# Performance work log

Hardware: AMD Instinct MI355X
Metric: run time of the kernel (lower is better)

## Reference

```python
import jax, jax.numpy as jnp
import numpy as np

EPS = 1e-5
K = 5  # sklearn NearestNeighbors(n_neighbors=5); includes the query point itself


def setup_inputs() -> dict:
    key = jax.random.key(0)
    points = jax.random.uniform(key, (16384, 3), dtype=jnp.float32)
    return {"points": points}


def _compute_lrfs(points):
    # Brute-force KNN (indices only; sklearn returns the self-point as nearest).
    sq = jnp.sum(points * points, axis=1)                      # [N]
    d2 = sq[:, None] + sq[None, :] - 2.0 * points @ points.T   # [N,N]
    _, nbh_idx = jax.lax.top_k(-jax.lax.stop_gradient(d2), K)  # [N,K] (indices only -> no grad path)

    diffs = points[nbh_idx] - points[:, None, :]               # [N,K,3]  (nbh = points[idx] - point)
    centered = diffs - diffs.mean(axis=1, keepdims=True)
    cov = jnp.einsum('nkd,nke->nde', centered, centered) / K   # torch.cov(nbh.T, correction=0)
    eigvals, eigvecs = jnp.linalg.eigh(cov)                    # ascending eigvals, [N,3],[N,3,3]
    order = jnp.argsort(eigvals, axis=-1)[:, ::-1]             # descending

    # NOTE faithful quirks of the original:
    #  - eigvecs.T[:, axis] == eigvecs[axis, :] -> ROW of eigvecs is used as the axis
    #  - _calc_axis receives nbh (already point-relative) and does (pt - point) again,
    #    so the vote uses (neighbor - 2*point) dotted with the axis.
    def axis_row(idx):
        v = jnp.take_along_axis(eigvecs, idx[:, None, None], axis=1)[:, 0, :]  # [N,3]
        vote_vec = diffs - points[:, None, :]                                  # [N,K,3]
        count = jnp.sum(jnp.einsum('nkd,nd->nk', vote_vec, v) >= -EPS, axis=1)
        sign = jnp.where(2 * count >= K, 1.0, -1.0).astype(points.dtype)       # count >= K/2 keeps
        return v * sign[:, None]

    x_axis = axis_row(order[:, 0])
    z_axis = axis_row(order[:, 2])
    y_axis = jnp.cross(z_axis, x_axis)
    return jnp.stack([x_axis, y_axis, z_axis], axis=1)  # [N,3,3]


def reference(points):
    # forward(points, return_lrfs=True) -> (shot=0, lrfs); return the lrfs (the only real output).
    return _compute_lrfs(points)
```

## Files before the change

kernel.cpp:

```cpp
#include <hip/hip_runtime.h>

#define SLARTG_NEW 1

namespace {

constexpr int KNN_K = 5;
constexpr int GRID = 16;
constexpr int CELLS = GRID * GRID * GRID;
constexpr int LPG = 8;

constexpr int PPB = 16;
constexpr int STR = 16;
constexpr int TPB = PPB * STR;
constexpr int TILE = 2048;

#define EPSF    5.9604644775390625e-8f
#define EPS2F   3.552713678800501e-15f
#define SAFMINF 1.1754943508222875e-38f
#define SAFMAXF 8.507059173023462e+37f
#define RTMINF  1.0842021724855044e-19f
#define RTMAXF  9.223372036854776e+18f

__device__ __forceinline__ float sqnorm3(float x, float y, float z) {
#pragma clang fp contract(off)
  float a = x * x;
  float b = y * y;
  float c = z * z;
  return (a + b) + c;
}

__device__ __forceinline__ float dist2(float xi, float yi, float zi, float sqi,
                                       float xj, float yj, float zj, float sqj) {
#pragma clang fp contract(off)
  float dot = (xi * xj + yi * yj) + zi * zj;
  float a = sqi + sqj;
  return a - 2.0f * dot;
}

__device__ __forceinline__ int cell1d(float v) {
  int c = (int)(v * (float)GRID);
  if (c < 0) c = 0;
  if (c > GRID - 1) c = GRID - 1;
  return c;
}

__device__ __forceinline__ float slapy2f(float x, float y) {
#pragma clang fp contract(off)
  float xa = fabsf(x), ya = fabsf(y);
  float w = fmaxf(xa, ya);
  float z = fminf(xa, ya);
  if (z == 0.f) return w;
  float q = z / w;
  float q2 = q * q;
  float s = 1.0f + q2;
  return w * sqrtf(s);
}

__device__ __forceinline__ void slartgf(float f, float g, float* cs, float* sn, float* r) {
#pragma clang fp contract(off)
#if SLARTG_NEW
  float f1 = fabsf(f), g1 = fabsf(g);
  if (g == 0.f) { *cs = 1.f; *sn = 0.f; *r = f; }
  else if (f == 0.f) { *cs = 0.f; *sn = copysignf(1.f, g); *r = g1; }
  else if (f1 > RTMINF && f1 < RTMAXF && g1 > RTMINF && g1 < RTMAXF) {
    float ff = f * f;
    float gg = g * g;
    float d = sqrtf(ff + gg);
    *cs = f1 / d;
    float rr = copysignf(d, f);
    *sn = g / rr;
    *r = rr;
  } else {
    float u = fminf(SAFMAXF, fmaxf(fmaxf(SAFMINF, f1), g1));
    float fs = f / u, gs = g / u;
    float ff = fs * fs;
    float gg = gs * gs;
    float d = sqrtf(ff + gg);
    *cs = fabsf(fs) / d;
    float rr = copysignf(d, f);
    *sn = gs / rr;
    *r = rr * u;
  }
#else
  if (g == 0.f) { *cs = 1.f; *sn = 0.f; *r = f; }
  else if (f == 0.f) { *cs = 0.f; *sn = 1.f; *r = g; }
  else {
    float f2 = f * f;
    float g2 = g * g;
    float rr = sqrtf(f2 + g2);
    float c = f / rr, s = g / rr;
    if (fabsf(f) > fabsf(g) && c < 0.f) { c = -c; s = -s; rr = -rr; }
    *cs = c; *sn = s; *r = rr;
  }
#endif
}

__device__ __forceinline__ void slaev2f(float a, float b, float c,
                                        float* rt1, float* rt2, float* cs1, float* sn1) {
#pragma clang fp contract(off)
  float sm = a + c;
  float df = a - c;
  float adf = fabsf(df);
  float tb = b + b;
  float ab = fabsf(tb);
  float acmx, acmn;
  if (fabsf(a) > fabsf(c)) { acmx = a; acmn = c; } else { acmx = c; acmn = a; }
  float rt;
  if (adf > ab) { float q = ab / adf; rt = adf * sqrtf(1.0f + q * q); }
  else if (adf < ab) { float q = adf / ab; rt = ab * sqrtf(1.0f + q * q); }
  else rt = ab * sqrtf(2.0f);
  int sgn1;
  if (sm < 0.f) { *rt1 = 0.5f * (sm - rt); sgn1 = -1; *rt2 = (acmx / *rt1) * acmn - (b / *rt1) * b; }
  else if (sm > 0.f) { *rt1 = 0.5f * (sm + rt); sgn1 = 1; *rt2 = (acmx / *rt1) * acmn - (b / *rt1) * b; }
  else { *rt1 = 0.5f * rt; *rt2 = -0.5f * rt; sgn1 = 1; }
  float cs; int sgn2;
  if (df >= 0.f) { cs = df + rt; sgn2 = 1; } else { cs = df - rt; sgn2 = -1; }
  float acs = fabsf(cs);
  float c1, s1;
  if (acs > ab) {
    float ct = -tb / cs;
    s1 = 1.0f / sqrtf(1.0f + ct * ct);
    c1 = ct * s1;
  } else {
    if (ab == 0.f) { c1 = 1.f; s1 = 0.f; }
    else {
      float tn = -cs / tb;
      c1 = 1.0f / sqrtf(1.0f + tn * tn);
      s1 = tn * c1;
    }
  }
  if (sgn1 == sgn2) { float tn = c1; c1 = -s1; s1 = tn; }
  *cs1 = c1; *sn1 = s1;
}

__device__ __forceinline__ void slascl_g(float cfrom, float cto, int n, float* a) {
#pragma clang fp contract(off)
  float cfromc = cfrom, ctoc = cto;
  bool done = false;
  int guard = 0;
  while (!done && guard++ < 50) {
    float mul;
    float cfrom1 = cfromc * SAFMINF;
    if (cfrom1 == cfromc) {
      mul = ctoc / cfromc; done = true;
    } else {
      float cto1 = ctoc / SAFMAXF;
      if (cto1 == ctoc) { mul = ctoc; done = true; cfromc = 1.f; }
      else if (fabsf(cfrom1) > fabsf(ctoc) && ctoc != 0.f) { mul = SAFMINF; done = false; cfromc = cfrom1; }
      else if (fabsf(cto1) > fabsf(cfromc)) { mul = SAFMAXF; done = false; ctoc = cto1; }
      else { mul = ctoc / cfromc; done = true; }
    }
    for (int i = 0; i < n; ++i) a[i] = a[i] * mul;
  }
}

__device__ void steqr3f(float* d, float* e, float Z[3][3]) {
#pragma clang fp contract(off)
  const int n = 3;
  const float eps = EPSF, eps2 = EPS2F, safmin = SAFMINF;
  const float ssfmax = sqrtf(SAFMAXF) / 3.0f;
  const float ssfmin = sqrtf(SAFMINF) / EPS2F;
  int jtot = 0; const int nmaxit = n * 30;
  int l1 = 1;

  for (int guard = 0; guard < 200; ++guard) {
    if (l1 > n) break;
    if (l1 > 1) e[l1 - 2] = 0.f;
    int m = n;
    if (l1 <= n - 1) {
      for (int q = l1; q <= n - 1; ++q) {
        float tst = fabsf(e[q - 1]);
        if (tst == 0.f) { m = q; break; }
        if (tst <= (sqrtf(fabsf(d[q - 1])) * sqrtf(fabsf(d[q]))) * eps) { e[q - 1] = 0.f; m = q; break; }
      }
    }
    int l = l1, lsv = l, lend = m, lendsv = lend;
    l1 = m + 1;
    if (lend == l) continue;
    float anorm = 0.f;
    for (int q = l; q <= lend; ++q) anorm = fmaxf(anorm, fabsf(d[q - 1]));
    for (int q = l; q <= lend - 1; ++q) anorm = fmaxf(anorm, fabsf(e[q - 1]));
    int iscale = 0;
    if (anorm == 0.f) continue;
    if (anorm > ssfmax) {
      iscale = 1;
      slascl_g(anorm, ssfmax, lend - l + 1, d + l - 1);
      slascl_g(anorm, ssfmax, lend - l, e + l - 1);
    } else if (anorm < ssfmin) {
      iscale = 2;
      slascl_g(anorm, ssfmin, lend - l + 1, d + l - 1);
      slascl_g(anorm, ssfmin, lend - l, e + l - 1);
    }
    if (fabsf(d[lend - 1]) < fabsf(d[l - 1])) { lend = lsv; l = lendsv; }

    if (lend > l) {
      for (int g2 = 0; g2 < 400; ++g2) {
        int mm = lend;
        if (l != lend) {
          bool fnd = false;
          for (int q = l; q <= lend - 1; ++q) {
            float tst = e[q - 1] * e[q - 1];
            if (tst <= (eps2 * fabsf(d[q - 1])) * fabsf(d[q]) + safmin) { mm = q; fnd = true; break; }
          }
          if (!fnd) mm = lend;
        }
        if (mm < lend) e[mm - 1] = 0.f;
        float p = d[l - 1];
        if (mm == l) {
          d[l - 1] = p; ++l;
          if (l <= lend) continue; else break;
        }
        if (mm == l + 1) {
          float rt1, rt2, c, s;
          slaev2f(d[l - 1], e[l - 1], d[l], &rt1, &rt2, &c, &s);
          for (int r2 = 0; r2 < 3; ++r2) {
            float zt = Z[r2][l];
            float zl = Z[r2][l - 1];
            Z[r2][l] = c * zt - s * zl;
            Z[r2][l - 1] = s * zt + c * zl;
          }
          d[l - 1] = rt1; d[l] = rt2; e[l - 1] = 0.f;
          l += 2;
          if (l <= lend) continue; else break;
        }
        if (jtot == nmaxit) break;
        ++jtot;
        float g = (d[l] - p) / (2.0f * e[l - 1]);
        float r = slapy2f(g, 1.0f);
        g = d[mm - 1] - p + e[l - 1] / (g + copysignf(r, g));
        float ss = 1.0f, cc = 1.0f;
        p = 0.f;
        float cw[2], sw[2];
        for (int q = mm - 1; q >= l; --q) {
          float f = ss * e[q - 1];
          float b = cc * e[q - 1];
          float rr;
          slartgf(g, f, &cc, &ss, &rr);
          if (q != mm - 1) e[q] = rr;
          g = d[q] - p;
          rr = (d[q - 1] - g) * ss + 2.0f * cc * b;
          p = ss * rr;
          d[q] = g + p;
          g = cc * rr - b;
          cw[q - l] = cc; sw[q - l] = -ss;
        }
        for (int q = mm - 1; q >= l; --q) {
          float cj = cw[q - l], sj = sw[q - l];
          for (int r2 = 0; r2 < 3; ++r2) {
            float zt = Z[r2][q];
            float zl = Z[r2][q - 1];
            Z[r2][q] = cj * zt - sj * zl;
            Z[r2][q - 1] = sj * zt + cj * zl;
          }
        }
        d[l - 1] = d[l - 1] - p;
        e[l - 1] = g;
      }
    } else {
      for (int g2 = 0; g2 < 400; ++g2) {
        int mm = lend;
        if (l != lend) {
          bool fnd = false;
          for (int q = l; q >= lend + 1; --q) {
            float tst = e[q - 2] * e[q - 2];
            if (tst <= (eps2 * fabsf(d[q - 1])) * fabsf(d[q - 2]) + safmin) { mm = q; fnd = true; break; }
          }
          if (!fnd) mm = lend;
        }
        if (mm > lend) e[mm - 2] = 0.f;
        float p = d[l - 1];
        if (mm == l) {
          d[l - 1] = p; --l;
          if (l >= lend) continue; else break;
        }
        if (mm == l - 1) {
          float rt1, rt2, c, s;
          slaev2f(d[l - 2], e[l - 2], d[l - 1], &rt1, &rt2, &c, &s);
          for (int r2 = 0; r2 < 3; ++r2) {
            float zt = Z[r2][l - 1];
            float zl = Z[r2][l - 2];
            Z[r2][l - 1] = c * zt - s * zl;
            Z[r2][l - 2] = s * zt + c * zl;
          }
          d[l - 2] = rt1; d[l - 1] = rt2; e[l - 2] = 0.f;
          l -= 2;
          if (l >= lend) continue; else break;
        }
        if (jtot == nmaxit) break;
        ++jtot;
        float g = (d[l - 2] - p) / (2.0f * e[l - 2]);
        float r = slapy2f(g, 1.0f);
        g = d[mm - 1] - p + e[l - 2] / (g + copysignf(r, g));
        float ss = 1.0f, cc = 1.0f;
        p = 0.f;
        float cw[2], sw[2];
        for (int q = mm; q <= l - 1; ++q) {
          float f = ss * e[q - 1];
          float b = cc * e[q - 1];
          float rr;
          slartgf(g, f, &cc, &ss, &rr);
          if (q != mm) e[q - 2] = rr;
          g = d[q - 1] - p;
          rr = (d[q] - g) * ss + 2.0f * cc * b;
          p = ss * rr;
          d[q - 1] = g + p;
          g = cc * rr - b;
          cw[q - mm] = cc; sw[q - mm] = ss;
        }
        for (int q = mm; q <= l - 1; ++q) {
          float cj = cw[q - mm], sj = sw[q - mm];
          for (int r2 = 0; r2 < 3; ++r2) {
            float zt = Z[r2][q];
            float zl = Z[r2][q - 1];
            Z[r2][q] = cj * zt - sj * zl;
            Z[r2][q - 1] = sj * zt + cj * zl;
          }
        }
        d[l - 1] = d[l - 1] - p;
        e[l - 2] = g;
      }
    }
    if (iscale == 1) {
      slascl_g(ssfmax, anorm, lendsv - lsv + 1, d + lsv - 1);
      slascl_g(ssfmax, anorm, lendsv - lsv, e + lsv - 1);
    } else if (iscale == 2) {
      slascl_g(ssfmin, anorm, lendsv - lsv + 1, d + lsv - 1);
      slascl_g(ssfmin, anorm, lendsv - lsv, e + lsv - 1);
    }
    if (jtot >= nmaxit) break;
  }
  for (int ii = 2; ii <= n; ++ii) {
    int i0 = ii - 1, k0 = i0;
    float p = d[i0 - 1];
    for (int j = ii; j <= n; ++j)
      if (d[j - 1] < p) { k0 = j; p = d[j - 1]; }
    if (k0 != i0) {
      d[k0 - 1] = d[i0 - 1]; d[i0 - 1] = p;
      for (int r2 = 0; r2 < 3; ++r2) {
        float t = Z[r2][i0 - 1]; Z[r2][i0 - 1] = Z[r2][k0 - 1]; Z[r2][k0 - 1] = t;
      }
    }
  }
}

__device__ __forceinline__ float vote5(const float dif[KNN_K][3],
                                       float px, float py, float pz, const float v[3]) {
#pragma clang fp contract(off)
  int cnt = 0;
  for (int k = 0; k < KNN_K; ++k) {
    float w0 = dif[k][0] - px;
    float w1 = dif[k][1] - py;
    float w2 = dif[k][2] - pz;
    float dt = (w0 * v[0] + w1 * v[1]) + w2 * v[2];
    cnt += (dt >= -1e-5f) ? 1 : 0;
  }
  return (2 * cnt >= KNN_K) ? 1.0f : -1.0f;
}

__device__ __forceinline__ void lrf_one(const float* __restrict__ P, float* __restrict__ out,
                                        int i, int n0, int n1, int n2, int n3, int n4) {
#pragma clang fp contract(off)
  int nb[KNN_K] = {n0, n1, n2, n3, n4};
  float px = P[i * 3 + 0], py = P[i * 3 + 1], pz = P[i * 3 + 2];
  float dif[KNN_K][3];
#pragma unroll
  for (int k = 0; k < KNN_K; ++k) {
    int j = nb[k];
    dif[k][0] = P[j * 3 + 0] - px;
    dif[k][1] = P[j * 3 + 1] - py;
    dif[k][2] = P[j * 3 + 2] - pz;
  }
  float mean[3];
  for (int c = 0; c < 3; ++c) {
    float sm = dif[0][c];
    for (int k = 1; k < KNN_K; ++k) sm = sm + dif[k][c];
    mean[c] = sm / 5.0f;
  }
  float cen[KNN_K][3];
  for (int k = 0; k < KNN_K; ++k)
    for (int c = 0; c < 3; ++c) cen[k][c] = dif[k][c] - mean[c];
  float cov[3][3];
  for (int a = 0; a < 3; ++a)
    for (int b = 0; b < 3; ++b) {
      float sm = cen[0][a] * cen[0][b];
      for (int k = 1; k < KNN_K; ++k) sm = sm + cen[k][a] * cen[k][b];
      cov[a][b] = sm / 5.0f;
    }

  float a00 = cov[0][0], a10 = cov[1][0], a20 = cov[2][0];
  float a11 = cov[1][1], a21 = cov[2][1], a22 = cov[2][2];
  float dd[3], ee[2];
  float taui = 0.f, v2 = 0.f;
  float xnorm = fabsf(a20);
  if (xnorm == 0.f) {
    taui = 0.f;
    ee[0] = a10;
    dd[0] = a00; dd[1] = a11; dd[2] = a22; ee[1] = a21;
  } else {
    float beta = -copysignf(slapy2f(a10, xnorm), a10);
    taui = (beta - a10) / beta;
    v2 = a20 * (1.0f / (a10 - beta));
    ee[0] = beta;
    float w1 = taui * a11 + taui * (a21 * v2);
    float w2 = taui * a21 + (taui * v2) * a22;
    float dot = w1 + w2 * v2;
    float al = -((0.5f * taui) * dot);
    w1 = w1 + al;
    w2 = w2 + al * v2;
    dd[1] = (a11 - w1) - w1;
    ee[1] = (a21 - (v2 * w1)) - w2;
    dd[2] = (a22 - (v2 * w2)) - (w2 * v2);
    dd[0] = a00;
  }

  float Zm[3][3] = {{1.f, 0.f, 0.f}, {0.f, 1.f, 0.f}, {0.f, 0.f, 1.f}};
  steqr3f(dd, ee, Zm);

  if (taui != 0.f) {
    for (int j = 0; j < 3; ++j) {
      float w = Zm[1][j] + v2 * Zm[2][j];
      float t = -(taui * w);
      Zm[1][j] = Zm[1][j] + t;
      Zm[2][j] = Zm[2][j] + v2 * t;
    }
  }

  float vx[3] = {Zm[2][0], Zm[2][1], Zm[2][2]};
  float vz[3] = {Zm[0][0], Zm[0][1], Zm[0][2]};
  float sx = vote5(dif, px, py, pz, vx);
  float sz = vote5(dif, px, py, pz, vz);
  float X[3] = {vx[0] * sx, vx[1] * sx, vx[2] * sx};
  float Zx[3] = {vz[0] * sz, vz[1] * sz, vz[2] * sz};
  float Y[3] = {Zx[1] * X[2] - Zx[2] * X[1],
                Zx[2] * X[0] - Zx[0] * X[2],
                Zx[0] * X[1] - Zx[1] * X[0]};
  out[i * 9 + 0] = X[0]; out[i * 9 + 1] = X[1]; out[i * 9 + 2] = X[2];
  out[i * 9 + 3] = Y[0]; out[i * 9 + 4] = Y[1]; out[i * 9 + 5] = Y[2];
  out[i * 9 + 6] = Zx[0]; out[i * 9 + 7] = Zx[1]; out[i * 9 + 8] = Zx[2];
}

__device__ __forceinline__ unsigned long long packkey(float d, int j) {
  unsigned int b = __float_as_uint(d);
  b ^= (b & 0x80000000u) ? 0xFFFFFFFFu : 0x80000000u;
  return ((unsigned long long)b << 32) | (unsigned int)j;
}

__device__ __forceinline__ float unpackd(unsigned long long k) {
  unsigned int b = (unsigned int)(k >> 32);
  b = (b & 0x80000000u) ? (b ^ 0x80000000u) : ~b;
  return __uint_as_float(b);
}

__device__ __forceinline__ int unpackj(unsigned long long k) {
  return (int)(unsigned int)(k & 0xFFFFFFFFu);
}

struct Key5 {
  unsigned long long k0, k1, k2, k3, k4;

  __device__ __forceinline__ void init() {
    k0 = k1 = k2 = k3 = k4 = 0xFFFFFFFFFFFFFFFFull;
  }

  __device__ __forceinline__ void insert(unsigned long long k) {
    if (k >= k4) return;
    bool l3 = k < k3;
    bool l2 = k < k2;
    bool l1 = k < k1;
    bool l0 = k < k0;
    k4 = l3 ? k3 : k;
    k3 = l3 ? (l2 ? k2 : k) : k3;
    k2 = l2 ? (l1 ? k1 : k) : k2;
    k1 = l1 ? (l0 ? k0 : k) : k1;
    k0 = l0 ? k : k0;
  }

  __device__ __forceinline__ void merge_xor(int off) {
    unsigned long long p0 = __shfl_xor(k0, off), p1 = __shfl_xor(k1, off),
                       p2 = __shfl_xor(k2, off), p3 = __shfl_xor(k3, off),
                       p4 = __shfl_xor(k4, off);
    insert(p0); insert(p1); insert(p2); insert(p3); insert(p4);
  }
};


__global__ __launch_bounds__(256) void hist_kernel(
    const float* __restrict__ P, int* __restrict__ counts, int n) {
  int i = blockIdx.x * 256 + threadIdx.x;
  if (i >= n) return;
  int cx = cell1d(P[i * 3 + 0]);
  int cy = cell1d(P[i * 3 + 1]);
  int cz = cell1d(P[i * 3 + 2]);
  atomicAdd(&counts[(cz * GRID + cy) * GRID + cx], 1);
}

__global__ __launch_bounds__(256) void scan_kernel(
    int* __restrict__ counts ,
    int* __restrict__ cursor) {
  __shared__ int psum[256];
  const int tid = threadIdx.x;
  const int CHUNK = CELLS / 256;
  int local[CHUNK];
  int s = 0;
  for (int k = 0; k < CHUNK; ++k) {
    local[k] = s;
    s += counts[tid * CHUNK + k];
  }
  psum[tid] = s;
  __syncthreads();
  for (int off = 1; off < 256; off <<= 1) {
    int v = (tid >= off) ? psum[tid - off] : 0;
    __syncthreads();
    psum[tid] += v;
    __syncthreads();
  }
  int base = (tid > 0) ? psum[tid - 1] : 0;
  for (int k = 0; k < CHUNK; ++k) {
    int o = base + local[k];
    counts[tid * CHUNK + k] = o;
    cursor[tid * CHUNK + k] = o;
  }
  if (tid == 255) counts[CELLS] = psum[255];
}

__global__ __launch_bounds__(256) void scatter_kernel(
    const float* __restrict__ P, int* __restrict__ cursor,
    float4* __restrict__ sorted, int n) {
  int i = blockIdx.x * 256 + threadIdx.x;
  if (i >= n) return;
  float x = P[i * 3 + 0], y = P[i * 3 + 1], z = P[i * 3 + 2];
  int c = (cell1d(z) * GRID + cell1d(y)) * GRID + cell1d(x);
  int pos = atomicAdd(&cursor[c], 1);
  sorted[pos] = make_float4(x, y, z, __int_as_float(i));
}

__global__ __launch_bounds__(256) void knn_kernel(
    const float4* __restrict__ sorted, const int* __restrict__ offsets,
    int* __restrict__ nbh, int n) {
  const int tid = threadIdx.x;
  const int r = tid & (LPG - 1);
  const int t = blockIdx.x * (256 / LPG) + (tid / LPG);
  if (t >= n) return;

  float4 q = sorted[t];
  const float qs = sqnorm3(q.x, q.y, q.z);
  const int cx = cell1d(q.x), cy = cell1d(q.y), cz = cell1d(q.z);
  const float h = 1.0f / (float)GRID;

  Key5 tp;
  tp.init();

  {
    const int x0 = max(0, cx - 1), x1 = min(GRID - 1, cx + 1);
    const int xsp = x1 - x0 + 1;
    int ksv[9], kev[9];
#pragma unroll
    for (int s9 = 0; s9 < 9; ++s9) {
      int dz = s9 / 3 - 1, dy = s9 % 3 - 1;
      int zz = cz + dz, yy = cy + dy;
      bool ok = (zz >= 0) && (zz < GRID) && (yy >= 0) && (yy < GRID);
      int c0 = ok ? ((zz * GRID + yy) * GRID + x0) : 0;
      int ks = offsets[c0];
      int ke = offsets[c0 + xsp];
      ksv[s9] = ks;
      kev[s9] = ok ? ke : ks;
    }
#pragma unroll
    for (int s9 = 0; s9 < 9; ++s9) {
      for (int k = ksv[s9] + r; k < kev[s9]; k += LPG) {
        float4 p = sorted[k];
        float psq = sqnorm3(p.x, p.y, p.z);
        float dv = dist2(q.x, q.y, q.z, qs, p.x, p.y, p.z, psq);
        tp.insert(packkey(dv, __float_as_int(p.w)));
      }
    }
  }

  float B = unpackd(tp.k4);
  B = fminf(B, __shfl_xor(B, 1));
  B = fminf(B, __shfl_xor(B, 2));
  B = fminf(B, __shfl_xor(B, 4));

  for (int m = 2; m < GRID; ++m) {
    float lb = (float)(m - 1) * h;
    if (lb * lb > B * 1.00001f + 1e-6f) break;
    for (int dz = -m; dz <= m; ++dz) {
      int zz = cz + dz;
      if (zz < 0 || zz >= GRID) continue;
      bool zface = (dz == -m || dz == m);
      for (int dy = -m; dy <= m; ++dy) {
        int yy = cy + dy;
        if (yy < 0 || yy >= GRID) continue;
        bool yface = (dy == -m || dy == m);
        int rowbase = (zz * GRID + yy) * GRID;
        if (zface || yface) {
          int x0 = max(0, cx - m), x1 = min(GRID - 1, cx + m);
          int ks = offsets[rowbase + x0], ke = offsets[rowbase + x1 + 1];
          for (int k = ks + r; k < ke; k += LPG) {
            float4 p = sorted[k];
            float psq = sqnorm3(p.x, p.y, p.z);
            float dv = dist2(q.x, q.y, q.z, qs, p.x, p.y, p.z, psq);
            tp.insert(packkey(dv, __float_as_int(p.w)));
          }
        } else {
          int xa = cx - m, xb = cx + m;
          if (xa >= 0) {
            int ks = offsets[rowbase + xa], ke = offsets[rowbase + xa + 1];
            for (int k = ks + r; k < ke; k += LPG) {
              float4 p = sorted[k];
              float psq = sqnorm3(p.x, p.y, p.z);
              float dv = dist2(q.x, q.y, q.z, qs, p.x, p.y, p.z, psq);
              tp.insert(packkey(dv, __float_as_int(p.w)));
            }
          }
          if (xb < GRID) {
            int ks = offsets[rowbase + xb], ke = offsets[rowbase + xb + 1];
            for (int k = ks + r; k < ke; k += LPG) {
              float4 p = sorted[k];
              float psq = sqnorm3(p.x, p.y, p.z);
              float dv = dist2(q.x, q.y, q.z, qs, p.x, p.y, p.z, psq);
              tp.insert(packkey(dv, __float_as_int(p.w)));
            }
          }
        }
      }
    }
    B = unpackd(tp.k4);
    B = fminf(B, __shfl_xor(B, 1));
    B = fminf(B, __shfl_xor(B, 2));
    B = fminf(B, __shfl_xor(B, 4));
  }

  tp.merge_xor(1);
  tp.merge_xor(2);
  tp.merge_xor(4);

  if (r == 0) {
    nbh[t * 5 + 0] = unpackj(tp.k0);
    nbh[t * 5 + 1] = unpackj(tp.k1);
    nbh[t * 5 + 2] = unpackj(tp.k2);
    nbh[t * 5 + 3] = unpackj(tp.k3);
    nbh[t * 5 + 4] = unpackj(tp.k4);
  }
}

__global__ __launch_bounds__(64) void solver_kernel(
    const float* __restrict__ P, const float4* __restrict__ sorted,
    const int* __restrict__ nbh, float* __restrict__ out, int n) {
  int t = blockIdx.x * 64 + threadIdx.x;
  if (t >= n) return;
  int io = __float_as_int(sorted[t].w);
  lrf_one(P, out, io,
          nbh[t * 5 + 0], nbh[t * 5 + 1], nbh[t * 5 + 2],
          nbh[t * 5 + 3], nbh[t * 5 + 4]);
}


__global__ __launch_bounds__(TPB) void knn_brute_kernel(
    const float* __restrict__ P, float* __restrict__ out, int n) {
  __shared__ float4 tile[TILE];

  const int tid = threadIdx.x;
  const int p = tid >> 4;
  const int s = tid & 15;
  const int i = blockIdx.x * PPB + p;
  const int iq = (i < n) ? i : (n - 1);

  const float qx = P[iq * 3 + 0];
  const float qy = P[iq * 3 + 1];
  const float qz = P[iq * 3 + 2];
  const float qs = sqnorm3(qx, qy, qz);

  Key5 t;
  t.init();

  for (int base = 0; base < n; base += TILE) {
    int cnt = min(TILE, n - base);
    __syncthreads();
    for (int j = tid; j < cnt; j += TPB) {
      float x = P[(base + j) * 3 + 0];
      float y = P[(base + j) * 3 + 1];
      float z = P[(base + j) * 3 + 2];
      tile[j] = make_float4(x, y, z, sqnorm3(x, y, z));
    }
    __syncthreads();
    for (int j = s; j < cnt; j += STR) {
      float4 q = tile[j];
      t.insert(packkey(dist2(qx, qy, qz, qs, q.x, q.y, q.z, q.w), base + j));
    }
  }

#pragma unroll
  for (int rnd = 0; rnd < 4; ++rnd) {
    t.merge_xor(1 << rnd);
  }

  if (s == 0 && i < n) {
    lrf_one(P, out, i, unpackj(t.k0), unpackj(t.k1), unpackj(t.k2),
            unpackj(t.k3), unpackj(t.k4));
  }
}

}

extern "C" void kernel_launch(void* const* d_in, const int* in_sizes, int n_in,
                              void* d_out, int out_size, void* d_ws, size_t ws_size,
                              hipStream_t stream) {
  (void)n_in; (void)out_size;
  const float* P = (const float*)d_in[0];
  float* out = (float*)d_out;
  const int n = in_sizes[0] / 3;
  if (n <= 0) return;

  size_t off_sorted = 0;
  size_t off_counts = off_sorted + (size_t)n * sizeof(float4);
  size_t off_cursor = off_counts + ((size_t)(CELLS + 1) * sizeof(int) + 15) / 16 * 16;
  size_t off_nbh = off_cursor + (size_t)CELLS * sizeof(int);
  size_t need = off_nbh + (size_t)n * 5 * sizeof(int);

  if (ws_size >= need && n >= KNN_K) {
    char* base = (char*)d_ws;
    float4* sorted = (float4*)(base + off_sorted);
    int* counts = (int*)(base + off_counts);
    int* cursor = (int*)(base + off_cursor);
    int* nbh = (int*)(base + off_nbh);

    hipMemsetAsync(counts, 0, (size_t)CELLS * sizeof(int), stream);
    hist_kernel<<<(n + 255) / 256, 256, 0, stream>>>(P, counts, n);
    scan_kernel<<<1, 256, 0, stream>>>(counts, cursor);
    scatter_kernel<<<(n + 255) / 256, 256, 0, stream>>>(P, cursor, sorted, n);
    const int ppb = 256 / LPG;
    knn_kernel<<<(n + ppb - 1) / ppb, 256, 0, stream>>>(sorted, counts, nbh, n);
    solver_kernel<<<(n + 63) / 64, 64, 0, stream>>>(P, sorted, nbh, out, n);
  } else {
    const int blocks = (n + PPB - 1) / PPB;
    knn_brute_kernel<<<blocks, TPB, 0, stream>>>(P, out, n);
  }
}
```

Before: 91.75 us.

## Classify points by eigensolver branch and reorder solver work to reduce divergence

Adds a classify kernel that recomputes the covariance tridiagonalization and predicts whether the QR or QL branch of the 3x3 eigensolver will be taken. It then builds a permutation with atomics so that threads in a wavefront follow the same path. The solver kernel runs in permuted order to cut warp divergence. This costs an extra kernel launch, a memset, redundant tridiagonal work, atomic contention and scattered gathers in the solver.

```diff
diff --git a/kernel.cpp b/kernel.cpp
--- a/kernel.cpp
+++ b/kernel.cpp
@@ -343,26 +343,12 @@
   }
 }
 
-__device__ __forceinline__ float vote5(const float dif[KNN_K][3],
-                                       float px, float py, float pz, const float v[3]) {
-#pragma clang fp contract(off)
-  int cnt = 0;
-  for (int k = 0; k < KNN_K; ++k) {
-    float w0 = dif[k][0] - px;
-    float w1 = dif[k][1] - py;
-    float w2 = dif[k][2] - pz;
-    float dt = (w0 * v[0] + w1 * v[1]) + w2 * v[2];
-    cnt += (dt >= -1e-5f) ? 1 : 0;
-  }
-  return (2 * cnt >= KNN_K) ? 1.0f : -1.0f;
-}
-
-__device__ __forceinline__ void lrf_one(const float* __restrict__ P, float* __restrict__ out,
-                                        int i, int n0, int n1, int n2, int n3, int n4) {
-#pragma clang fp contract(off)
-  int nb[KNN_K] = {n0, n1, n2, n3, n4};
+__device__ __forceinline__ void tridiag_of(const float* __restrict__ P, int i,
+                                           const int* nb, float dif[KNN_K][3],
+                                           float dd[3], float ee[2],
+                                           float* taui_o, float* v2_o) {
+#pragma clang fp contract(off)
   float px = P[i * 3 + 0], py = P[i * 3 + 1], pz = P[i * 3 + 2];
-  float dif[KNN_K][3];
 #pragma unroll
   for (int k = 0; k < KNN_K; ++k) {
     int j = nb[k];
@@ -389,7 +375,6 @@
 
   float a00 = cov[0][0], a10 = cov[1][0], a20 = cov[2][0];
   float a11 = cov[1][1], a21 = cov[2][1], a22 = cov[2][2];
-  float dd[3], ee[2];
   float taui = 0.f, v2 = 0.f;
   float xnorm = fabsf(a20);
   if (xnorm == 0.f) {
@@ -412,9 +397,36 @@
     dd[2] = (a22 - (v2 * w2)) - (w2 * v2);
     dd[0] = a00;
   }
+  *taui_o = taui;
+  *v2_o = v2;
+}
+
+__device__ __forceinline__ float vote5(const float dif[KNN_K][3],
+                                       float px, float py, float pz, const float v[3]) {
+#pragma clang fp contract(off)
+  int cnt = 0;
+  for (int k = 0; k < KNN_K; ++k) {
+    float w0 = dif[k][0] - px;
+    float w1 = dif[k][1] - py;
+    float w2 = dif[k][2] - pz;
+    float dt = (w0 * v[0] + w1 * v[1]) + w2 * v[2];
+    cnt += (dt >= -1e-5f) ? 1 : 0;
+  }
+  return (2 * cnt >= KNN_K) ? 1.0f : -1.0f;
+}
+
+__device__ __forceinline__ void lrf_one(const float* __restrict__ P, float* __restrict__ out,
+                                        int i, int n0, int n1, int n2, int n3, int n4) {
+#pragma clang fp contract(off)
+  int nb[KNN_K] = {n0, n1, n2, n3, n4};
+  float dif[KNN_K][3];
+  float dd[3], ee3[3];
+  float taui, v2;
+  tridiag_of(P, i, nb, dif, dd, ee3, &taui, &v2);
+  ee3[2] = 0.f;
 
   float Zm[3][3] = {{1.f, 0.f, 0.f}, {0.f, 1.f, 0.f}, {0.f, 0.f, 1.f}};
-  steqr3f(dd, ee, Zm);
+  steqr3f(dd, ee3, Zm);
 
   if (taui != 0.f) {
     for (int j = 0; j < 3; ++j) {
@@ -425,6 +437,7 @@
     }
   }
 
+  float px = P[i * 3 + 0], py = P[i * 3 + 1], pz = P[i * 3 + 2];
   float vx[3] = {Zm[2][0], Zm[2][1], Zm[2][2]};
   float vz[3] = {Zm[0][0], Zm[0][1], Zm[0][2]};
   float sx = vote5(dif, px, py, pz, vx);
@@ -644,11 +657,48 @@
   }
 }
 
+__global__ __launch_bounds__(256) void classify_kernel(
+    const float* __restrict__ P, const float4* __restrict__ sorted,
+    const int* __restrict__ nbh, int* __restrict__ perm,
+    int* __restrict__ cnts, int n) {
+#pragma clang fp contract(off)
+  int t = blockIdx.x * 256 + threadIdx.x;
+  if (t >= n) return;
+  int io = __float_as_int(sorted[t].w);
+  int nb[KNN_K] = {nbh[t * 5 + 0], nbh[t * 5 + 1], nbh[t * 5 + 2],
+                   nbh[t * 5 + 3], nbh[t * 5 + 4]};
+  float dif[KNN_K][3];
+  float dd[3], ee[2];
+  float taui, v2;
+  tridiag_of(P, io, nb, dif, dd, ee, &taui, &v2);
+
+  const float eps = EPSF;
+  int m = 3;
+  for (int q = 1; q <= 2; ++q) {
+    float tst = fabsf(ee[q - 1]);
+    if (tst == 0.f) { m = q; break; }
+    if (tst <= (sqrtf(fabsf(dd[q - 1])) * sqrtf(fabsf(dd[q]))) * eps) { m = q; break; }
+  }
+  bool qr = false;
+  if (m > 1) {
+    qr = (fabsf(dd[m - 1]) < fabsf(dd[0]));
+  }
+  if (qr) {
+    int pos = atomicAdd(&cnts[1], 1);
+    perm[n - 1 - pos] = t;
+  } else {
+    int pos = atomicAdd(&cnts[0], 1);
+    perm[pos] = t;
+  }
+}
+
 __global__ __launch_bounds__(64) void solver_kernel(
     const float* __restrict__ P, const float4* __restrict__ sorted,
-    const int* __restrict__ nbh, float* __restrict__ out, int n) {
-  int t = blockIdx.x * 64 + threadIdx.x;
-  if (t >= n) return;
+    const int* __restrict__ nbh, const int* __restrict__ perm,
+    float* __restrict__ out, int n) {
+  int s = blockIdx.x * 64 + threadIdx.x;
+  if (s >= n) return;
+  int t = perm[s];
   int io = __float_as_int(sorted[t].w);
   lrf_one(P, out, io,
           nbh[t * 5 + 0], nbh[t * 5 + 1], nbh[t * 5 + 2],
@@ -716,7 +766,9 @@
   size_t off_counts = off_sorted + (size_t)n * sizeof(float4);
   size_t off_cursor = off_counts + ((size_t)(CELLS + 1) * sizeof(int) + 15) / 16 * 16;
   size_t off_nbh = off_cursor + (size_t)CELLS * sizeof(int);
-  size_t need = off_nbh + (size_t)n * 5 * sizeof(int);
+  size_t off_perm = off_nbh + (size_t)n * 5 * sizeof(int);
+  size_t off_cnts = off_perm + (size_t)n * sizeof(int);
+  size_t need = off_cnts + 16;
 
   if (ws_size >= need && n >= KNN_K) {
     char* base = (char*)d_ws;
@@ -724,14 +776,18 @@
     int* counts = (int*)(base + off_counts);
     int* cursor = (int*)(base + off_cursor);
     int* nbh = (int*)(base + off_nbh);
+    int* perm = (int*)(base + off_perm);
+    int* cnts = (int*)(base + off_cnts);
 
     hipMemsetAsync(counts, 0, (size_t)CELLS * sizeof(int), stream);
+    hipMemsetAsync(cnts, 0, 2 * sizeof(int), stream);
     hist_kernel<<<(n + 255) / 256, 256, 0, stream>>>(P, counts, n);
     scan_kernel<<<1, 256, 0, stream>>>(counts, cursor);
     scatter_kernel<<<(n + 255) / 256, 256, 0, stream>>>(P, cursor, sorted, n);
     const int ppb = 256 / LPG;
     knn_kernel<<<(n + ppb - 1) / ppb, 256, 0, stream>>>(sorted, counts, nbh, n);
-    solver_kernel<<<(n + 63) / 64, 64, 0, stream>>>(P, sorted, nbh, out, n);
+    classify_kernel<<<(n + 255) / 256, 256, 0, stream>>>(P, sorted, nbh, perm, cnts, n);
+    solver_kernel<<<(n + 63) / 64, 64, 0, stream>>>(P, sorted, nbh, perm, out, n);
   } else {
     const int blocks = (n + PPB - 1) / PPB;
     knn_brute_kernel<<<blocks, TPB, 0, stream>>>(P, out, n);
```

New measurement: 91.66 us, median of 2. Within noise of the previous version (-0.1%).
